# Kernel tuning notes

Hardware: AMD Instinct MI355X
Metric: run time of the kernel (lower is better)

Reference implementation:

```python
import jax, jax.numpy as jnp
import numpy as np

EPS_NORM = 1e-8   # torch cosine_similarity norm eps
EPS_DEN = 1e-10
CLAMP_MAX = 1e10


def _cos_matrix(a, b):
    # rows of a vs rows of b: [Na, Nb] cosine similarity via normalized matmul
    an = a / jnp.clip(jnp.linalg.norm(a, axis=-1, keepdims=True), EPS_NORM)
    bn = b / jnp.clip(jnp.linalg.norm(b, axis=-1, keepdims=True), EPS_NORM)
    return an @ bn.T


def setup_inputs() -> dict:
    key = jax.random.key(0)
    k1, k2, k3, k4, k5 = jax.random.split(key, 5)
    N, D, M, C = 4096, 256, 2, 100
    return {
        "label_encodings": jax.random.normal(k1, (N, D), dtype=jnp.float32),
        "fusion_z": jax.random.normal(k2, (M, N, D), dtype=jnp.float32),
        "sample_embeddings": jax.random.normal(k3, (N, D), dtype=jnp.float32),
        "label_embeddings": jax.random.normal(k4, (N, D), dtype=jnp.float32),
        "labels": jax.random.randint(k5, (N,), 0, C, dtype=jnp.int64),
        "temperature": jnp.ones((), dtype=jnp.float32),
        "xi": jnp.ones((), dtype=jnp.float32),
    }


def reference(label_encodings, fusion_z, sample_embeddings, label_embeddings,
              labels, temperature, xi):
    # ---- class_prompt_contrastive_Learning ----
    sim = _cos_matrix(label_encodings, label_encodings)            # [N, N]
    e = jnp.minimum(jnp.exp(sim / temperature), CLAMP_MAX)
    mask = (labels[:, None] == labels[None, :])
    num = jnp.sum(e * mask, axis=1)
    den = jnp.clip(jnp.sum(e, axis=1), EPS_DEN)
    loss_class = jnp.mean(-jnp.log(num / den))

    # ---- supervised_cross_view_contrastive ----
    M, N, D = fusion_z.shape
    fz = fusion_z.reshape(M * N, D)
    lab_exp = jnp.tile(labels, M)                                  # labels.repeat(M)
    mask2 = (lab_exp[:, None] == lab_exp[None, :])
    sim2 = _cos_matrix(fz, fz)                                     # [MN, MN]
    e2 = jnp.exp(sim2 / temperature)
    num2 = jnp.sum(e2 * mask2, axis=1)
    den2 = jnp.clip(jnp.sum(e2, axis=1), EPS_DEN)
    loss_cross = jnp.mean(-jnp.log(num2 / den2))

    # ---- boundary_aware_independent_hashing ----
    cs = _cos_matrix(sample_embeddings, label_embeddings)          # [N, N]
    Dm = (1.0 - cs) * 0.5
    y = (labels[:, None] == labels[None, :]).astype(cs.dtype)
    loss_mat = y * Dm ** 2 + (1.0 - y) * jnp.maximum(xi - Dm, 0.0) ** 2
    loss_hash = jnp.mean(loss_mat)

    return jnp.stack([loss_class, loss_cross, loss_hash])
```

## Files before the change

kernel.cpp:

```cpp
#include <hip/hip_runtime.h>
#include <hip/hip_bf16.h>
#include <stdint.h>


typedef __attribute__((ext_vector_type(8))) short bf16x8;
typedef __attribute__((ext_vector_type(4))) float f32x4;

__device__ inline void gload_lds16(const void* g, void* l) {
  __builtin_amdgcn_global_load_lds(
      (__attribute__((address_space(1))) void*)g,
      (__attribute__((address_space(3))) void*)l, 16, 0, 0);
}

__device__ inline void barrier_raw() {
  asm volatile("" ::: "memory");
  __builtin_amdgcn_s_barrier();
  asm volatile("" ::: "memory");
}

__device__ inline void lgkm_barrier() {
  asm volatile("s_waitcnt lgkmcnt(0)" ::: "memory");
  __builtin_amdgcn_s_barrier();
  asm volatile("" ::: "memory");
}

__device__ inline unsigned short f2bf(float x) {
  unsigned int u = __builtin_bit_cast(unsigned int, x);
  u = (u + 0x7fffu + ((u >> 16) & 1u)) >> 16;
  return (unsigned short)u;
}

__global__ __launch_bounds__(256) void norm_kernel(
    const float* __restrict__ LE, const float* __restrict__ FZ,
    const float* __restrict__ SE, const float* __restrict__ LM,
    unsigned short* __restrict__ An, unsigned short* __restrict__ Fn,
    unsigned short* __restrict__ Sn, unsigned short* __restrict__ Ln,
    float* __restrict__ hacc, float* __restrict__ out) {
  const int tid = threadIdx.x;
  if (blockIdx.x == 0) {
    if (tid == 0) out[0] = 0.f;
    if (tid == 1) out[1] = 0.f;
    if (tid == 2) hacc[0] = 0.f;
  }

  const int wid = tid >> 6, lane = tid & 63;
  const int row = blockIdx.x * 4 + wid;

  const float* src;
  unsigned short* dst;
  int r;
  if (row < 4096)       { src = LE; dst = An; r = row; }
  else if (row < 12288) { src = FZ; dst = Fn; r = row - 4096; }
  else if (row < 16384) { src = SE; dst = Sn; r = row - 12288; }
  else                  { src = LM; dst = Ln; r = row - 16384; }

  const float4 v = *(const float4*)(src + (size_t)r * 256 + lane * 4);
  float ss = v.x * v.x + v.y * v.y + v.z * v.z + v.w * v.w;
#pragma unroll
  for (int m = 1; m < 64; m <<= 1) ss += __shfl_xor(ss, m);
  const float scale = 1.0f / fmaxf(sqrtf(ss), 1e-8f);

  ushort4 o;
  o.x = f2bf(v.x * scale);
  o.y = f2bf(v.y * scale);
  o.z = f2bf(v.z * scale);
  o.w = f2bf(v.w * scale);
  *(ushort4*)(dst + (size_t)r * 256 + lane * 4) = o;
}

__device__ inline void tri_decode(int t, int nb, int& rb, int& cb) {
  int r = 0;
  while (t >= nb - r) { t -= nb - r; ++r; }
  rb = r;
  cb = r + t;
}

__device__ inline void decode_tile(
    int bid, const unsigned short* An, const unsigned short* Fn,
    const unsigned short* Sn, const unsigned short* Ln, int& mode, int& rb,
    int& cb, const unsigned short*& X, const unsigned short*& Y) {
  if (bid < 528) {
    mode = 0; tri_decode(bid, 32, rb, cb); X = An; Y = An;
  } else if (bid < 2608) {
    mode = 1; tri_decode(bid - 528, 64, rb, cb); X = Fn; Y = Fn;
  } else {
    mode = 2; const int t = bid - 2608; rb = t >> 5; cb = t & 31;
    X = Sn; Y = Ln;
  }
}

__global__ __launch_bounds__(512, 4) void fused_sim(
    const unsigned short* __restrict__ An, const unsigned short* __restrict__ Fn,
    const unsigned short* __restrict__ Sn, const unsigned short* __restrict__ Ln,
    const int* __restrict__ labels,
    const float* __restrict__ tp, const float* __restrict__ xip,
    float2* __restrict__ Pc,
    float2* __restrict__ Px,
    float* __restrict__ hacc) {
  __shared__ __align__(16) char Ab[2][16384];
  __shared__ __align__(16) char Bb[2][16384];
  __shared__ int lrS[128], lcS[128];
  __shared__ float sN[256], sD[256], cN[512], cD[512];

  const int tid = threadIdx.x;
  const int lane = tid & 63, wid = tid >> 6;
  const int wr = wid >> 1, wc = wid & 1;
  const int g = lane >> 4, c = lane & 15;

  const int hw = blockIdx.x;
  int bid = (hw & 7) * 64 + (hw >> 3);

  const int srow = tid >> 3;
  const int sgl = (tid & 7) ^ (srow & 7);
  const int pxs = c & 7;
  const int aoff = (wr * 32 + c) * 128;
  const int boff = (wc * 64 + c) * 128;

  const float invt = 1.0f / tp[0];
  const float xi = xip[0];

  int mode, rb, cb;
  const unsigned short *X, *Y;
  decode_tile(bid, An, Fn, Sn, Ln, mode, rb, cb, X, Y);
  const char* xs = (const char*)X + ((size_t)rb * 128 + srow) * 512 + sgl * 16;
  const char* ys = (const char*)Y + ((size_t)cb * 128 + srow) * 512 + sgl * 16;

#define STAGE(PX, PY, KK, BUF)                                            \
  do {                                                                    \
    const char* xa = (PX) + (KK) * 128;                                   \
    const char* ya = (PY) + (KK) * 128;                                   \
    char* da = (char*)(&Ab[(BUF)][0]) + wid * 1024;                       \
    char* db = (char*)(&Bb[(BUF)][0]) + wid * 1024;                       \
    gload_lds16(xa, da);                                                  \
    gload_lds16(xa + 32768, da + 8192);                                   \
    gload_lds16(ya, db);                                                  \
    gload_lds16(ya + 32768, db + 8192);                                   \
  } while (0)

  int mylab =
      labels[(tid < 128 ? rb * 128 + tid : cb * 128 + tid - 128) & 4095];
  STAGE(xs, ys, 0, 0);
  STAGE(xs, ys, 1, 1);
  asm volatile("" : "+v"(mylab));

  f32x4 acc[2][4];
  const f32x4 zero = {0.f, 0.f, 0.f, 0.f};

  while (true) {
    const int nbid = bid + 512;
    const bool has_next = (nbid < 3632);
    int nmode = 0, nrb = 0, ncb = 0;
    const unsigned short *nX = nullptr, *nY = nullptr;
    const char *nxs = nullptr, *nys = nullptr;
    if (has_next) {
      decode_tile(nbid, An, Fn, Sn, Ln, nmode, nrb, ncb, nX, nY);
      nxs = (const char*)nX + ((size_t)nrb * 128 + srow) * 512 + sgl * 16;
      nys = (const char*)nY + ((size_t)ncb * 128 + srow) * 512 + sgl * 16;
    }

#pragma unroll
    for (int m = 0; m < 2; ++m)
#pragma unroll
      for (int n = 0; n < 4; ++n) acc[m][n] = zero;

#pragma unroll
    for (int kk = 0; kk < 4; ++kk) {
      if (kk == 3 && !has_next) {
        asm volatile("s_waitcnt vmcnt(0)" ::: "memory");
      } else {
        asm volatile("s_waitcnt vmcnt(4)" ::: "memory");
      }
      barrier_raw();
      if (kk == 0) {
        if (tid < 128)      lrS[tid] = mylab;
        else if (tid < 256) lcS[tid - 128] = mylab;
      }
      const char* ab = (const char*)(&Ab[kk & 1][0]) + aoff;
      const char* bb = (const char*)(&Bb[kk & 1][0]) + boff;
#pragma unroll
      for (int ks = 0; ks < 2; ++ks) {
        const int px = ((ks * 4 + g) ^ pxs) * 16;
        bf16x8 af[2], bg[4];
#pragma unroll
        for (int m = 0; m < 2; ++m)
          af[m] = *(const bf16x8*)(ab + m * 2048 + px);
#pragma unroll
        for (int n = 0; n < 4; ++n)
          bg[n] = *(const bf16x8*)(bb + n * 2048 + px);
        __builtin_amdgcn_s_setprio(1);
#pragma unroll
        for (int m = 0; m < 2; ++m)
#pragma unroll
          for (int n = 0; n < 4; ++n)
            acc[m][n] = __builtin_amdgcn_mfma_f32_16x16x32_bf16(
                af[m], bg[n], acc[m][n], 0, 0, 0);
        __builtin_amdgcn_s_setprio(0);
      }
      barrier_raw();
      if (kk < 2) {
        STAGE(xs, ys, kk + 2, kk & 1);
      } else if (kk == 2 && has_next) {
        mylab = labels[(tid < 128 ? nrb * 128 + tid : ncb * 128 + tid - 128) &
                       4095];
        STAGE(nxs, nys, 0, 0);
        asm volatile("" : "+v"(mylab));
      }
    }
    if (has_next) STAGE(nxs, nys, 1, 1);

    if (mode < 2) {
      const bool docol = (rb != cb);
      float2* Pp = (mode == 0) ? Pc : Px;
      const int NR = (mode == 0) ? 4096 : 8192;
      int collab[4];
#pragma unroll
      for (int n = 0; n < 4; ++n) collab[n] = lcS[wc * 64 + n * 16 + c];

      float cn[4] = {0.f, 0.f, 0.f, 0.f}, cd[4] = {0.f, 0.f, 0.f, 0.f};
      float rn[8], rd[8];
#pragma unroll
      for (int m = 0; m < 2; ++m) {
#pragma unroll
        for (int reg = 0; reg < 4; ++reg) {
          const int rlab = lrS[wr * 32 + m * 16 + g * 4 + reg];
          float pn = 0.f, pd = 0.f;
#pragma unroll
          for (int n = 0; n < 4; ++n) {
            float e = __expf(acc[m][n][reg] * invt);
            if (mode == 0) e = fminf(e, 1e10f);
            pd += e;
            const float en = (rlab == collab[n]) ? e : 0.f;
            pn += en;
            cd[n] += e;
            cn[n] += en;
          }
#pragma unroll
          for (int msk = 1; msk < 16; msk <<= 1) {
            pn += __shfl_xor(pn, msk);
            pd += __shfl_xor(pd, msk);
          }
          rn[m * 4 + reg] = pn;
          rd[m * 4 + reg] = pd;
        }
      }
      if (c == 0) {
#pragma unroll
        for (int m = 0; m < 2; ++m)
#pragma unroll
          for (int reg = 0; reg < 4; ++reg) {
            const int rloc = wr * 32 + m * 16 + g * 4 + reg;
            sN[wc * 128 + rloc] = rn[m * 4 + reg];
            sD[wc * 128 + rloc] = rd[m * 4 + reg];
          }
      }
#pragma unroll
      for (int n = 0; n < 4; ++n) {
        float a = cn[n], b = cd[n];
        a += __shfl_xor(a, 16); b += __shfl_xor(b, 16);
        a += __shfl_xor(a, 32); b += __shfl_xor(b, 32);
        if (g == 0) {
          cN[wr * 128 + wc * 64 + n * 16 + c] = a;
          cD[wr * 128 + wc * 64 + n * 16 + c] = b;
        }
      }
      lgkm_barrier();
      if (tid < 128) {
        Pp[(size_t)cb * NR + rb * 128 + tid] =
            make_float2(sN[tid] + sN[128 + tid], sD[tid] + sD[128 + tid]);
      } else if (tid < 256 && docol) {
        const int t2 = tid - 128;
        Pp[(size_t)rb * NR + cb * 128 + t2] = make_float2(
            cN[t2] + cN[128 + t2] + cN[256 + t2] + cN[384 + t2],
            cD[t2] + cD[128 + t2] + cD[256 + t2] + cD[384 + t2]);
      }
    } else {
      int collab[4];
#pragma unroll
      for (int n = 0; n < 4; ++n) collab[n] = lcS[wc * 64 + n * 16 + c];
      float part = 0.f;
#pragma unroll
      for (int m = 0; m < 2; ++m)
#pragma unroll
        for (int reg = 0; reg < 4; ++reg) {
          const int rlab = lrS[wr * 32 + m * 16 + g * 4 + reg];
#pragma unroll
          for (int n = 0; n < 4; ++n) {
            const float cs = acc[m][n][reg];
            const float Dm = (1.0f - cs) * 0.5f;
            const float u = fmaxf(xi - Dm, 0.0f);
            part += (rlab == collab[n]) ? Dm * Dm : u * u;
          }
        }
#pragma unroll
      for (int msk = 1; msk < 64; msk <<= 1) part += __shfl_xor(part, msk);
      if (lane == 0) sN[wid] = part;
      lgkm_barrier();
      if (tid == 0) {
        float s = 0.f;
#pragma unroll
        for (int w = 0; w < 8; ++w) s += sN[w];
        atomicAdd(hacc, s);
      }
    }

    if (!has_next) break;
    bid = nbid; mode = nmode; rb = nrb; cb = ncb;
    xs = nxs; ys = nys;
  }
#undef STAGE
}

__global__ __launch_bounds__(256) void finalize_kernel(
    const float2* __restrict__ Pc, const float2* __restrict__ Px,
    const float* __restrict__ hacc, float* __restrict__ out) {
  const int b = blockIdx.x, tid = threadIdx.x;
  const float2* P;
  int nslots, NR, row, oi;
  if (b < 16) { P = Pc; nslots = 32; NR = 4096; row = b * 256 + tid; oi = 0; }
  else { P = Px; nslots = 64; NR = 8192; row = (b - 16) * 256 + tid; oi = 1; }
  float n = 0.f, d = 0.f;
  for (int s = 0; s < nslots; ++s) {
    const float2 v = P[(size_t)s * NR + row];
    n += v.x;
    d += v.y;
  }
  float val = -logf(n / fmaxf(d, 1e-10f));
#pragma unroll
  for (int m = 1; m < 64; m <<= 1) val += __shfl_xor(val, m);
  __shared__ float r[4];
  if ((tid & 63) == 0) r[tid >> 6] = val;
  __syncthreads();
  if (tid == 0) atomicAdd(&out[oi], (r[0] + r[1] + r[2] + r[3]) / (float)NR);
  if (b == 0 && tid == 0) out[2] = hacc[0] * (1.0f / 16777216.0f);
}

extern "C" void kernel_launch(void* const* d_in, const int* in_sizes, int n_in,
                              void* d_out, int out_size, void* d_ws,
                              size_t ws_size, hipStream_t stream) {
  const float* LE = (const float*)d_in[0];
  const float* FZ = (const float*)d_in[1];
  const float* SE = (const float*)d_in[2];
  const float* LM = (const float*)d_in[3];
  const int* labels = (const int*)d_in[4];
  const float* tp = (const float*)d_in[5];
  const float* xip = (const float*)d_in[6];
  float* out = (float*)d_out;

  char* ws = (char*)d_ws;
  unsigned short* An = (unsigned short*)(ws);
  unsigned short* Fn = (unsigned short*)(ws + 2097152);
  unsigned short* Sn = (unsigned short*)(ws + 6291456);
  unsigned short* Ln = (unsigned short*)(ws + 8388608);
  float2* Pc = (float2*)(ws + 10485760);
  float2* Px = (float2*)(ws + 11534336);
  float* hacc = (float*)(ws + 15728640);

  norm_kernel<<<dim3(5120), dim3(256), 0, stream>>>(LE, FZ, SE, LM, An, Fn,
                                                    Sn, Ln, hacc, out);
  fused_sim<<<dim3(512), dim3(512), 0, stream>>>(An, Fn, Sn, Ln, labels, tp,
                                                 xip, Pc, Px, hacc);
  finalize_kernel<<<dim3(48), dim3(256), 0, stream>>>(Pc, Px, hacc, out);
}
```

Measured before the change: 172.7 us.

## Use 128-wide K stages, contiguous per-block tile ranges, and async label staging

The K-chunk per pipeline stage doubles from 64 to 128, so each tile runs two stages instead of four and hits fewer barriers. LDS buffers grow to 64KB each, with a 16-way swizzle to match. The persistent grid halves to 256 blocks, and each block walks a contiguous range of tile indices assigned per XCD instead of a strided schedule, which should improve L2 locality. Labels are now loaded into double-buffered LDS through async global-to-LDS loads, but occupancy drops (launch bounds 4→2 blocks) and fewer blocks may leave CUs idle.

```diff
diff --git a/kernel.cpp b/kernel.cpp
--- a/kernel.cpp
+++ b/kernel.cpp
@@ -89,7 +89,7 @@
   }
 }
 
-__global__ __launch_bounds__(512, 4) void fused_sim(
+__global__ __launch_bounds__(512, 2) void fused_sim(
     const unsigned short* __restrict__ An, const unsigned short* __restrict__ Fn,
     const unsigned short* __restrict__ Sn, const unsigned short* __restrict__ Ln,
     const int* __restrict__ labels,
@@ -97,9 +97,9 @@
     float2* __restrict__ Pc,
     float2* __restrict__ Px,
     float* __restrict__ hacc) {
-  __shared__ __align__(16) char Ab[2][16384];
-  __shared__ __align__(16) char Bb[2][16384];
-  __shared__ int lrS[128], lcS[128];
+  __shared__ __align__(16) char Ab[2][32768];
+  __shared__ __align__(16) char Bb[2][32768];
+  __shared__ __align__(16) int labS[2][256];
   __shared__ float sN[256], sD[256], cN[512], cD[512];
 
   const int tid = threadIdx.x;
@@ -108,52 +108,83 @@
   const int g = lane >> 4, c = lane & 15;
 
   const int hw = blockIdx.x;
-  int bid = (hw & 7) * 64 + (hw >> 3);
-
-  const int srow = tid >> 3;
-  const int sgl = (tid & 7) ^ (srow & 7);
-  const int pxs = c & 7;
-  const int aoff = (wr * 32 + c) * 128;
-  const int boff = (wc * 64 + c) * 128;
+  const int xcd = hw & 7, slot = hw >> 3;
+  int ti = xcd * 454 + slot * 14 + (slot < 6 ? slot : 6);
+  const int tend = ti + 14 + (slot < 6 ? 1 : 0);
+
+  const int srow = tid >> 4;
+  const int sgl = (tid & 15) ^ (srow & 15);
+  const int pxs = c;
+  const int aoff = (wr * 32 + c) * 256;
+  const int boff = (wc * 64 + c) * 256;
 
   const float invt = 1.0f / tp[0];
   const float xi = xip[0];
 
-  int mode, rb, cb;
-  const unsigned short *X, *Y;
-  decode_tile(bid, An, Fn, Sn, Ln, mode, rb, cb, X, Y);
-  const char* xs = (const char*)X + ((size_t)rb * 128 + srow) * 512 + sgl * 16;
-  const char* ys = (const char*)Y + ((size_t)cb * 128 + srow) * 512 + sgl * 16;
-
-#define STAGE(PX, PY, KK, BUF)                                            \
+#define STAGE_T(PX, PY, KH, BUF)                                          \
   do {                                                                    \
-    const char* xa = (PX) + (KK) * 128;                                   \
-    const char* ya = (PY) + (KK) * 128;                                   \
+    const char* xa = (PX) + (KH) * 256;                                   \
+    const char* ya = (PY) + (KH) * 256;                                   \
     char* da = (char*)(&Ab[(BUF)][0]) + wid * 1024;                       \
     char* db = (char*)(&Bb[(BUF)][0]) + wid * 1024;                       \
     gload_lds16(xa, da);                                                  \
-    gload_lds16(xa + 32768, da + 8192);                                   \
+    gload_lds16(xa + 16384, da + 8192);                                   \
+    gload_lds16(xa + 32768, da + 16384);                                  \
+    gload_lds16(xa + 49152, da + 24576);                                  \
     gload_lds16(ya, db);                                                  \
-    gload_lds16(ya + 32768, db + 8192);                                   \
+    gload_lds16(ya + 16384, db + 8192);                                   \
+    gload_lds16(ya + 32768, db + 16384);                                  \
+    gload_lds16(ya + 49152, db + 24576);                                  \
   } while (0)
 
-  int mylab =
-      labels[(tid < 128 ? rb * 128 + tid : cb * 128 + tid - 128) & 4095];
-  STAGE(xs, ys, 0, 0);
-  STAGE(xs, ys, 1, 1);
-  asm volatile("" : "+v"(mylab));
-
+#define STAGE_LAB(RB, CB, PAR)                                            \
+  do {                                                                    \
+    const int pb = (lane < 32 ? (RB) : (CB)) * 512;                       \
+    const char* ls = (const char*)labels + (pb & 16383) + (lane & 31) * 16; \
+    gload_lds16(ls, (char*)(&labS[(PAR)][0]));                            \
+  } while (0)
+
+#define COMPUTE(BUF)                                                      \
+  do {                                                                    \
+    const char* ab = (const char*)(&Ab[(BUF)][0]) + aoff;                 \
+    const char* bb = (const char*)(&Bb[(BUF)][0]) + boff;                 \
+    _Pragma("unroll") for (int ks = 0; ks < 4; ++ks) {                    \
+      const int px = ((ks * 4 + g) ^ pxs) * 16;                           \
+      bf16x8 af[2], bg[4];                                                \
+      _Pragma("unroll") for (int m = 0; m < 2; ++m)                       \
+          af[m] = *(const bf16x8*)(ab + m * 4096 + px);                   \
+      _Pragma("unroll") for (int n = 0; n < 4; ++n)                       \
+          bg[n] = *(const bf16x8*)(bb + n * 4096 + px);                   \
+      __builtin_amdgcn_s_setprio(1);                                      \
+      _Pragma("unroll") for (int m = 0; m < 2; ++m)                       \
+          _Pragma("unroll") for (int n = 0; n < 4; ++n)                   \
+              acc[m][n] = __builtin_amdgcn_mfma_f32_16x16x32_bf16(        \
+                  af[m], bg[n], acc[m][n], 0, 0, 0);                      \
+      __builtin_amdgcn_s_setprio(0);                                      \
+    }                                                                     \
+  } while (0)
+
+  int mode, rb, cb;
+  const unsigned short *X, *Y;
+  decode_tile(ti, An, Fn, Sn, Ln, mode, rb, cb, X, Y);
+  const char* xs = (const char*)X + ((size_t)rb * 128 + srow) * 512 + sgl * 16;
+  const char* ys = (const char*)Y + ((size_t)cb * 128 + srow) * 512 + sgl * 16;
+
+  STAGE_LAB(rb, cb, 0);
+  STAGE_T(xs, ys, 0, 0);
+  STAGE_T(xs, ys, 1, 1);
+
+  int par = 0;
   f32x4 acc[2][4];
   const f32x4 zero = {0.f, 0.f, 0.f, 0.f};
 
   while (true) {
-    const int nbid = bid + 512;
-    const bool has_next = (nbid < 3632);
+    const bool has_next = (ti + 1 < tend);
     int nmode = 0, nrb = 0, ncb = 0;
     const unsigned short *nX = nullptr, *nY = nullptr;
     const char *nxs = nullptr, *nys = nullptr;
     if (has_next) {
-      decode_tile(nbid, An, Fn, Sn, Ln, nmode, nrb, ncb, nX, nY);
+      decode_tile(ti + 1, An, Fn, Sn, Ln, nmode, nrb, ncb, nX, nY);
       nxs = (const char*)nX + ((size_t)nrb * 128 + srow) * 512 + sgl * 16;
       nys = (const char*)nY + ((size_t)ncb * 128 + srow) * 512 + sgl * 16;
     }
@@ -163,151 +194,129 @@
 #pragma unroll
       for (int n = 0; n < 4; ++n) acc[m][n] = zero;
 
-#pragma unroll
-    for (int kk = 0; kk < 4; ++kk) {
-      if (kk == 3 && !has_next) {
-        asm volatile("s_waitcnt vmcnt(0)" ::: "memory");
+    asm volatile("s_waitcnt vmcnt(8)" ::: "memory");
+    barrier_raw();
+    COMPUTE(0);
+    barrier_raw();
+    if (has_next) {
+      STAGE_LAB(nrb, ncb, par ^ 1);
+      STAGE_T(nxs, nys, 0, 0);
+    }
+
+    if (has_next) asm volatile("s_waitcnt vmcnt(9)" ::: "memory");
+    else          asm volatile("s_waitcnt vmcnt(0)" ::: "memory");
+    barrier_raw();
+    COMPUTE(1);
+    barrier_raw();
+
+    {
+      const int* lrS = &labS[par][0];
+      const int* lcS = &labS[par][128];
+      if (mode < 2) {
+        const bool docol = (rb != cb);
+        float2* Pp = (mode == 0) ? Pc : Px;
+        const int NR = (mode == 0) ? 4096 : 8192;
+        int collab[4];
+#pragma unroll
+        for (int n = 0; n < 4; ++n) collab[n] = lcS[wc * 64 + n * 16 + c];
+
+        float cn[4] = {0.f, 0.f, 0.f, 0.f}, cd[4] = {0.f, 0.f, 0.f, 0.f};
+        float rn[8], rd[8];
+#pragma unroll
+        for (int m = 0; m < 2; ++m) {
+#pragma unroll
+          for (int reg = 0; reg < 4; ++reg) {
+            const int rlab = lrS[wr * 32 + m * 16 + g * 4 + reg];
+            float pn = 0.f, pd = 0.f;
+#pragma unroll
+            for (int n = 0; n < 4; ++n) {
+              float e = __expf(acc[m][n][reg] * invt);
+              if (mode == 0) e = fminf(e, 1e10f);
+              pd += e;
+              const float en = (rlab == collab[n]) ? e : 0.f;
+              pn += en;
+              cd[n] += e;
+              cn[n] += en;
+            }
+#pragma unroll
+            for (int msk = 1; msk < 16; msk <<= 1) {
+              pn += __shfl_xor(pn, msk);
+              pd += __shfl_xor(pd, msk);
+            }
+            rn[m * 4 + reg] = pn;
+            rd[m * 4 + reg] = pd;
+          }
+        }
+        if (c == 0) {
+#pragma unroll
+          for (int m = 0; m < 2; ++m)
+#pragma unroll
+            for (int reg = 0; reg < 4; ++reg) {
+              const int rloc = wr * 32 + m * 16 + g * 4 + reg;
+              sN[wc * 128 + rloc] = rn[m * 4 + reg];
+              sD[wc * 128 + rloc] = rd[m * 4 + reg];
+            }
+        }
+#pragma unroll
+        for (int n = 0; n < 4; ++n) {
+          float a = cn[n], b = cd[n];
+          a += __shfl_xor(a, 16); b += __shfl_xor(b, 16);
+          a += __shfl_xor(a, 32); b += __shfl_xor(b, 32);
+          if (g == 0) {
+            cN[wr * 128 + wc * 64 + n * 16 + c] = a;
+            cD[wr * 128 + wc * 64 + n * 16 + c] = b;
+          }
+        }
+        lgkm_barrier();
+        if (tid < 128) {
+          Pp[(size_t)cb * NR + rb * 128 + tid] =
+              make_float2(sN[tid] + sN[128 + tid], sD[tid] + sD[128 + tid]);
+        } else if (tid < 256 && docol) {
+          const int t2 = tid - 128;
+          Pp[(size_t)rb * NR + cb * 128 + t2] = make_float2(
+              cN[t2] + cN[128 + t2] + cN[256 + t2] + cN[384 + t2],
+              cD[t2] + cD[128 + t2] + cD[256 + t2] + cD[384 + t2]);
+        }
       } else {
-        asm volatile("s_waitcnt vmcnt(4)" ::: "memory");
-      }
-      barrier_raw();
-      if (kk == 0) {
-        if (tid < 128)      lrS[tid] = mylab;
-        else if (tid < 256) lcS[tid - 128] = mylab;
-      }
-      const char* ab = (const char*)(&Ab[kk & 1][0]) + aoff;
-      const char* bb = (const char*)(&Bb[kk & 1][0]) + boff;
-#pragma unroll
-      for (int ks = 0; ks < 2; ++ks) {
-        const int px = ((ks * 4 + g) ^ pxs) * 16;
-        bf16x8 af[2], bg[4];
+        int collab[4];
+#pragma unroll
+        for (int n = 0; n < 4; ++n) collab[n] = lcS[wc * 64 + n * 16 + c];
+        float part = 0.f;
 #pragma unroll
         for (int m = 0; m < 2; ++m)
-          af[m] = *(const bf16x8*)(ab + m * 2048 + px);
-#pragma unroll
-        for (int n = 0; n < 4; ++n)
-          bg[n] = *(const bf16x8*)(bb + n * 2048 + px);
-        __builtin_amdgcn_s_setprio(1);
-#pragma unroll
-        for (int m = 0; m < 2; ++m)
-#pragma unroll
-          for (int n = 0; n < 4; ++n)
-            acc[m][n] = __builtin_amdgcn_mfma_f32_16x16x32_bf16(
-                af[m], bg[n], acc[m][n], 0, 0, 0);
-        __builtin_amdgcn_s_setprio(0);
-      }
-      barrier_raw();
-      if (kk < 2) {
-        STAGE(xs, ys, kk + 2, kk & 1);
-      } else if (kk == 2 && has_next) {
-        mylab = labels[(tid < 128 ? nrb * 128 + tid : ncb * 128 + tid - 128) &
-                       4095];
-        STAGE(nxs, nys, 0, 0);
-        asm volatile("" : "+v"(mylab));
+#pragma unroll
+          for (int reg = 0; reg < 4; ++reg) {
+            const int rlab = lrS[wr * 32 + m * 16 + g * 4 + reg];
+#pragma unroll
+            for (int n = 0; n < 4; ++n) {
+              const float cs = acc[m][n][reg];
+              const float Dm = (1.0f - cs) * 0.5f;
+              const float u = fmaxf(xi - Dm, 0.0f);
+              part += (rlab == collab[n]) ? Dm * Dm : u * u;
+            }
+          }
+#pragma unroll
+        for (int msk = 1; msk < 64; msk <<= 1) part += __shfl_xor(part, msk);
+        if (lane == 0) sN[wid] = part;
+        lgkm_barrier();
+        if (tid == 0) {
+          float s = 0.f;
+#pragma unroll
+          for (int w = 0; w < 8; ++w) s += sN[w];
+          atomicAdd(hacc, s);
+        }
+        lgkm_barrier();
       }
     }
-    if (has_next) STAGE(nxs, nys, 1, 1);
-
-    if (mode < 2) {
-      const bool docol = (rb != cb);
-      float2* Pp = (mode == 0) ? Pc : Px;
-      const int NR = (mode == 0) ? 4096 : 8192;
-      int collab[4];
-#pragma unroll
-      for (int n = 0; n < 4; ++n) collab[n] = lcS[wc * 64 + n * 16 + c];
-
-      float cn[4] = {0.f, 0.f, 0.f, 0.f}, cd[4] = {0.f, 0.f, 0.f, 0.f};
-      float rn[8], rd[8];
-#pragma unroll
-      for (int m = 0; m < 2; ++m) {
-#pragma unroll
-        for (int reg = 0; reg < 4; ++reg) {
-          const int rlab = lrS[wr * 32 + m * 16 + g * 4 + reg];
-          float pn = 0.f, pd = 0.f;
-#pragma unroll
-          for (int n = 0; n < 4; ++n) {
-            float e = __expf(acc[m][n][reg] * invt);
-            if (mode == 0) e = fminf(e, 1e10f);
-            pd += e;
-            const float en = (rlab == collab[n]) ? e : 0.f;
-            pn += en;
-            cd[n] += e;
-            cn[n] += en;
-          }
-#pragma unroll
-          for (int msk = 1; msk < 16; msk <<= 1) {
-            pn += __shfl_xor(pn, msk);
-            pd += __shfl_xor(pd, msk);
-          }
-          rn[m * 4 + reg] = pn;
-          rd[m * 4 + reg] = pd;
-        }
-      }
-      if (c == 0) {
-#pragma unroll
-        for (int m = 0; m < 2; ++m)
-#pragma unroll
-          for (int reg = 0; reg < 4; ++reg) {
-            const int rloc = wr * 32 + m * 16 + g * 4 + reg;
-            sN[wc * 128 + rloc] = rn[m * 4 + reg];
-            sD[wc * 128 + rloc] = rd[m * 4 + reg];
-          }
-      }
-#pragma unroll
-      for (int n = 0; n < 4; ++n) {
-        float a = cn[n], b = cd[n];
-        a += __shfl_xor(a, 16); b += __shfl_xor(b, 16);
-        a += __shfl_xor(a, 32); b += __shfl_xor(b, 32);
-        if (g == 0) {
-          cN[wr * 128 + wc * 64 + n * 16 + c] = a;
-          cD[wr * 128 + wc * 64 + n * 16 + c] = b;
-        }
-      }
-      lgkm_barrier();
-      if (tid < 128) {
-        Pp[(size_t)cb * NR + rb * 128 + tid] =
-            make_float2(sN[tid] + sN[128 + tid], sD[tid] + sD[128 + tid]);
-      } else if (tid < 256 && docol) {
-        const int t2 = tid - 128;
-        Pp[(size_t)rb * NR + cb * 128 + t2] = make_float2(
-            cN[t2] + cN[128 + t2] + cN[256 + t2] + cN[384 + t2],
-            cD[t2] + cD[128 + t2] + cD[256 + t2] + cD[384 + t2]);
-      }
-    } else {
-      int collab[4];
-#pragma unroll
-      for (int n = 0; n < 4; ++n) collab[n] = lcS[wc * 64 + n * 16 + c];
-      float part = 0.f;
-#pragma unroll
-      for (int m = 0; m < 2; ++m)
-#pragma unroll
-        for (int reg = 0; reg < 4; ++reg) {
-          const int rlab = lrS[wr * 32 + m * 16 + g * 4 + reg];
-#pragma unroll
-          for (int n = 0; n < 4; ++n) {
-            const float cs = acc[m][n][reg];
-            const float Dm = (1.0f - cs) * 0.5f;
-            const float u = fmaxf(xi - Dm, 0.0f);
-            part += (rlab == collab[n]) ? Dm * Dm : u * u;
-          }
-        }
-#pragma unroll
-      for (int msk = 1; msk < 64; msk <<= 1) part += __shfl_xor(part, msk);
-      if (lane == 0) sN[wid] = part;
-      lgkm_barrier();
-      if (tid == 0) {
-        float s = 0.f;
-#pragma unroll
-        for (int w = 0; w < 8; ++w) s += sN[w];
-        atomicAdd(hacc, s);
-      }
-    }
 
     if (!has_next) break;
-    bid = nbid; mode = nmode; rb = nrb; cb = ncb;
-    xs = nxs; ys = nys;
+    STAGE_T(nxs, nys, 1, 1);
+    ++ti; par ^= 1;
+    mode = nmode; rb = nrb; cb = ncb; xs = nxs; ys = nys;
   }
-#undef STAGE
+#undef STAGE_T
+#undef STAGE_LAB
+#undef COMPUTE
 }
 
 __global__ __launch_bounds__(256) void finalize_kernel(
@@ -357,7 +366,7 @@
 
   norm_kernel<<<dim3(5120), dim3(256), 0, stream>>>(LE, FZ, SE, LM, An, Fn,
                                                     Sn, Ln, hacc, out);
-  fused_sim<<<dim3(512), dim3(512), 0, stream>>>(An, Fn, Sn, Ln, labels, tp,
+  fused_sim<<<dim3(256), dim3(512), 0, stream>>>(An, Fn, Sn, Ln, labels, tp,
                                                  xip, Pc, Px, hacc);
   finalize_kernel<<<dim3(48), dim3(256), 0, stream>>>(Pc, Px, hacc, out);
 }
```

After: 190.4 us. +10.3%, slower.
